# Kernel tuning notes

Measured on AMD Instinct MI355X. Metric: run time of the kernel, lower is better.

The kernel has to match this reference:

```python
import jax, jax.numpy as jnp
import numpy as np
from jax import lax

B, H, W = 1024, 28, 28
STEPS, KMAX = 32, 2
OUT_F, NUM_CLASSES = 32, 10
P = H * W  # 784 flattened filtration values
TSEQ1 = jnp.linspace(0.01, 0.29, STEPS, dtype=jnp.float32)
TSEQ2 = jnp.linspace(0.05, 0.3, STEPS, dtype=jnp.float32)
DN = ('NHWC', 'HWIO', 'NHWC')


def setup_inputs() -> dict:
    key = jax.random.key(0)
    ks = jax.random.split(key, 16)
    return {
        'x': jax.random.normal(ks[0], (B, H, W, 1), jnp.float32),
        'x_dtm005': jax.random.uniform(ks[1], (B, H, W, 1), jnp.float32, 0.0, 0.3),
        'x_dtm02': jax.random.uniform(ks[2], (B, H, W, 1), jnp.float32, 0.0, 0.3),
        'conv_w1': jax.random.normal(ks[3], (3, 3, 1, 32), jnp.float32) * 0.1,
        'conv_b1': jnp.zeros((32,), jnp.float32),
        'conv_w2': jax.random.normal(ks[4], (3, 3, 32, 1), jnp.float32) * 0.1,
        'conv_b2': jnp.zeros((1,), jnp.float32),
        'g1_w': jax.random.normal(ks[5], (KMAX * STEPS, OUT_F), jnp.float32) * 0.1,
        'g1_b': jnp.zeros((OUT_F,), jnp.float32),
        'g2_w': jax.random.normal(ks[6], (KMAX * STEPS, OUT_F), jnp.float32) * 0.1,
        'g2_b': jnp.zeros((OUT_F,), jnp.float32),
        'fc1_w': jax.random.normal(ks[7], (P + 2 * OUT_F, 64), jnp.float32) * 0.05,
        'fc1_b': jnp.zeros((64,), jnp.float32),
        'fc2_w': jax.random.normal(ks[8], (64, NUM_CLASSES), jnp.float32) * 0.1,
        'fc2_b': jnp.zeros((NUM_CLASSES,), jnp.float32),
    }


def _landscape(v, tseq):
    """Persistence landscape over a grid of t-values.

    v: [B, P] filtration (DTM) values; each value is a birth time, paired
    with a per-sample death at the max filtration value (sublevel sweep).
    Landscape lambda_k(t) = k-th largest tent max(0, min(t-b, d-t)).
    Returns [B, KMAX*STEPS].
    """
    death = jnp.max(v, axis=1)                                     # [B]
    # tent: [B, T, P]
    tent = jnp.maximum(0.0, jnp.minimum(tseq[None, :, None] - v[:, None, :],
                                        death[:, None, None] - tseq[None, :, None]))
    top = lax.top_k(tent, KMAX)[0]                                 # [B, T, K]
    return jnp.transpose(top, (0, 2, 1)).reshape(v.shape[0], KMAX * tseq.shape[0])


def reference(x, x_dtm005, x_dtm02, conv_w1, conv_b1, conv_w2, conv_b2,
              g1_w, g1_b, g2_w, g2_b, fc1_w, fc1_b, fc2_w, fc2_b):
    b = x.shape[0]
    # TDA branch 1 (sublevel=True -> no negation)
    x1 = _landscape(x_dtm005.reshape(b, -1), TSEQ1)
    x1 = jax.nn.relu(x1 @ g1_w + g1_b)
    # TDA branch 2
    x2 = _landscape(x_dtm02.reshape(b, -1), TSEQ2)
    x2 = jax.nn.relu(x2 @ g2_w + g2_b)
    # CNN branch: Conv(32) -> ReLU -> Conv(1), then extra ReLU per call()
    h = lax.conv_general_dilated(x, conv_w1, (1, 1), 'SAME', dimension_numbers=DN) + conv_b1
    h = jax.nn.relu(h)
    h = lax.conv_general_dilated(h, conv_w2, (1, 1), 'SAME', dimension_numbers=DN) + conv_b2
    h = jax.nn.relu(h)
    hf = h.reshape(b, -1)                                          # [B, 784]
    z = jnp.concatenate([hf, x1, x2], axis=-1)                     # [B, 848]
    z = jax.nn.relu(z @ fc1_w + fc1_b)
    return z @ fc2_w + fc2_b                                       # [B, 10]
```

## Files before the change

### kernel.cpp

```cpp
#include <hip/hip_runtime.h>

#define BATCH 1024
#define PP 784

__global__ __launch_bounds__(256) void fused_kernel(
    const float* __restrict__ xin,
    const float* __restrict__ dtm1, const float* __restrict__ dtm2,
    const float* __restrict__ w1g, const float* __restrict__ b1g,
    const float* __restrict__ w2g, const float* __restrict__ b2g,
    const float* __restrict__ g1w, const float* __restrict__ g1b,
    const float* __restrict__ g2w, const float* __restrict__ g2b,
    const float* __restrict__ fc1w, const float* __restrict__ fc1b,
    const float* __restrict__ fc2w, const float* __restrict__ fc2b,
    float* __restrict__ out)
{
  const int b = blockIdx.x;
  const int tid = threadIdx.x;
  const int lane = tid & 63;
  const int w = tid >> 6;
  const int x = lane & 31;
  const int sub = lane >> 5;

  __shared__ float inL[28][36];
  __shared__ float w1L[9][32];
  __shared__ float w2L[9][32];
  __shared__ float b1L[32];
  __shared__ float pL[4][28][28];
  __shared__ __align__(16) float zL[864];
  __shared__ float red[2][4][3];
  __shared__ float fin[2][3];
  __shared__ float pfc[4][64];
  __shared__ float z1L[64];

  float4 tv1, tv2;
  if (tid < 196) {
    tv1 = *(const float4*)&dtm1[b * PP + tid * 4];
    tv2 = *(const float4*)&dtm2[b * PP + tid * 4];
  }

  for (int i = tid; i < 224; i += 256) {
    int y = i >> 3, k = i & 7;
    inL[y][k == 0 ? 0 : 28 + k] = 0.f;
  }
  for (int i = tid; i < 784; i += 256)
    inL[i / 28][i % 28 + 1] = xin[b * PP + i];
  for (int i = tid; i < 288; i += 256) {
    ((float*)w1L)[i] = w1g[i];
    ((float*)w2L)[i] = w2g[i];
  }
  if (tid < 32) b1L[tid] = b1g[tid];
  __syncthreads();

  float acc[28];
#pragma unroll
  for (int y = 0; y < 28; ++y) acc[y] = 0.f;

#pragma unroll 1
  for (int cp = 0; cp < 4; ++cp) {
    const int c = (w << 3) + (cp << 1) + sub;
    float wa[9], wb[9];
#pragma unroll
    for (int t = 0; t < 9; ++t) { wa[t] = w1L[t][c]; wb[t] = w2L[t][c]; }
    const float bb = b1L[c];

    float ra0 = 0.f, ra1 = 0.f, ra2 = 0.f;
    float rb0 = inL[0][x], rb1 = inL[0][x + 1], rb2 = inL[0][x + 2];

#pragma unroll
    for (int y = 0; y < 28; ++y) {
      float rc0, rc1, rc2;
      if (y + 1 < 28) {
        rc0 = inL[y + 1][x]; rc1 = inL[y + 1][x + 1]; rc2 = inL[y + 1][x + 2];
      } else {
        rc0 = 0.f; rc1 = 0.f; rc2 = 0.f;
      }
      float h = bb;
      h = fmaf(ra0, wa[0], h); h = fmaf(ra1, wa[1], h); h = fmaf(ra2, wa[2], h);
      h = fmaf(rb0, wa[3], h); h = fmaf(rb1, wa[4], h); h = fmaf(rb2, wa[5], h);
      h = fmaf(rc0, wa[6], h); h = fmaf(rc1, wa[7], h); h = fmaf(rc2, wa[8], h);
      h = (x < 28) ? fmaxf(h, 0.f) : 0.f;
      float hl = __shfl_up(h, 1, 32);  hl = (x == 0) ? 0.f : hl;
      float hr = __shfl_down(h, 1, 32);
      if (y + 1 < 28) {
        acc[y + 1] = fmaf(hl, wb[0], acc[y + 1]);
        acc[y + 1] = fmaf(h , wb[1], acc[y + 1]);
        acc[y + 1] = fmaf(hr, wb[2], acc[y + 1]);
      }
      acc[y] = fmaf(hl, wb[3], acc[y]);
      acc[y] = fmaf(h , wb[4], acc[y]);
      acc[y] = fmaf(hr, wb[5], acc[y]);
      if (y > 0) {
        acc[y - 1] = fmaf(hl, wb[6], acc[y - 1]);
        acc[y - 1] = fmaf(h , wb[7], acc[y - 1]);
        acc[y - 1] = fmaf(hr, wb[8], acc[y - 1]);
      }
      ra0 = rb0; ra1 = rb1; ra2 = rb2;
      rb0 = rc0; rb1 = rc1; rb2 = rc2;
    }
  }
#pragma unroll
  for (int y = 0; y < 28; ++y) acc[y] += __shfl_xor(acc[y], 32);
  if (sub == 0 && x < 28) {
#pragma unroll
    for (int y = 0; y < 28; ++y) pL[w][y][x] = acc[y];
  }
  __syncthreads();

  {
    const float b2v = b2g[0];
    const float* pw = (const float*)pL;
    for (int u = tid; u < 784; u += 256) {
      float v = pw[u] + pw[784 + u] + pw[1568 + u] + pw[2352 + u] + b2v;
      zL[u] = fmaxf(v, 0.f);
    }
  }
#pragma unroll
  for (int br = 0; br < 2; ++br) {
    float m1 = 1e30f, m2 = 1e30f, mx = -1e30f;
    if (tid < 196) {
      float4 x4 = br ? tv2 : tv1;
      float xs[4] = {x4.x, x4.y, x4.z, x4.w};
#pragma unroll
      for (int k = 0; k < 4; ++k) {
        float v = xs[k];
        mx = fmaxf(mx, v);
        float nm1 = fminf(m1, v);
        m2 = fminf(m2, fmaxf(m1, v));
        m1 = nm1;
      }
    }
#pragma unroll
    for (int off = 32; off >= 1; off >>= 1) {
      float o1 = __shfl_xor(m1, off);
      float o2 = __shfl_xor(m2, off);
      float ox = __shfl_xor(mx, off);
      mx = fmaxf(mx, ox);
      float nm1 = fminf(m1, o1);
      m2 = fminf(fminf(m2, o2), fmaxf(m1, o1));
      m1 = nm1;
    }
    if ((tid & 63) == 0) {
      red[br][w][0] = m1; red[br][w][1] = m2; red[br][w][2] = mx;
    }
  }
  __syncthreads();
  if (tid < 2) {
    float m1 = 1e30f, m2 = 1e30f, mx = -1e30f;
#pragma unroll
    for (int wv = 0; wv < 4; ++wv) {
      float o1 = red[tid][wv][0], o2 = red[tid][wv][1], ox = red[tid][wv][2];
      mx = fmaxf(mx, ox);
      float nm1 = fminf(m1, o1);
      m2 = fminf(fminf(m2, o2), fmaxf(m1, o1));
      m1 = nm1;
    }
    fin[tid][0] = m1; fin[tid][1] = m2; fin[tid][2] = mx;
  }
  __syncthreads();
  if (tid < 64) {
    const int br = tid >> 5, j = tid & 31;
    const float m1 = fin[br][0], m2 = fin[br][1], mx = fin[br][2];
    const float* gw = br ? g2w : g1w;
    const float* gb = br ? g2b : g1b;
    const float t0 = br ? 0.05f : 0.01f;
    const float dt = br ? (0.25f / 31.0f) : (0.28f / 31.0f);
    float a = gb[j];
#pragma unroll 4
    for (int i = 0; i < 64; ++i) {
      const int k = i >> 5, ti = i & 31;
      float tv = t0 + dt * (float)ti;
      float vk = k ? m2 : m1;
      float lam = fmaxf(0.0f, fminf(tv - vk, mx - tv));
      a = fmaf(lam, gw[i * 32 + j], a);
    }
    zL[784 + br * 32 + j] = fmaxf(a, 0.0f);
  }
  __syncthreads();

  {
    const int j = tid & 63, part = tid >> 6;
    float a = 0.f;
    const int i0 = part * 212;
#pragma unroll 4
    for (int i = i0; i < i0 + 212; i += 4) {
      float4 z4 = *(float4*)&zL[i];
      a = fmaf(z4.x, fc1w[(i + 0) * 64 + j], a);
      a = fmaf(z4.y, fc1w[(i + 1) * 64 + j], a);
      a = fmaf(z4.z, fc1w[(i + 2) * 64 + j], a);
      a = fmaf(z4.w, fc1w[(i + 3) * 64 + j], a);
    }
    pfc[part][j] = a;
  }
  __syncthreads();
  if (tid < 64) {
    float v = pfc[0][tid] + pfc[1][tid] + pfc[2][tid] + pfc[3][tid] + fc1b[tid];
    z1L[tid] = fmaxf(v, 0.f);
  }
  __syncthreads();
  if (tid < 10) {
    float a = fc2b[tid];
#pragma unroll 8
    for (int jj = 0; jj < 64; ++jj)
      a = fmaf(z1L[jj], fc2w[jj * 10 + tid], a);
    out[b * 10 + tid] = a;
  }
}

extern "C" void kernel_launch(void* const* d_in, const int* in_sizes, int n_in,
                              void* d_out, int out_size, void* d_ws, size_t ws_size,
                              hipStream_t stream) {
  const float* x       = (const float*)d_in[0];
  const float* dtm005  = (const float*)d_in[1];
  const float* dtm02   = (const float*)d_in[2];
  const float* conv_w1 = (const float*)d_in[3];
  const float* conv_b1 = (const float*)d_in[4];
  const float* conv_w2 = (const float*)d_in[5];
  const float* conv_b2 = (const float*)d_in[6];
  const float* g1_w    = (const float*)d_in[7];
  const float* g1_b    = (const float*)d_in[8];
  const float* g2_w    = (const float*)d_in[9];
  const float* g2_b    = (const float*)d_in[10];
  const float* fc1_w   = (const float*)d_in[11];
  const float* fc1_b   = (const float*)d_in[12];
  const float* fc2_w   = (const float*)d_in[13];
  const float* fc2_b   = (const float*)d_in[14];
  float* out = (float*)d_out;

  fused_kernel<<<BATCH, 256, 0, stream>>>(
      x, dtm005, dtm02, conv_w1, conv_b1, conv_w2, conv_b2,
      g1_w, g1_b, g2_w, g2_b, fc1_w, fc1_b, fc2_w, fc2_b, out);
}
```

Before: 128.5 us.

## Restructure fused conv to stream rows with rolling accumulators and DPP shifts

```diff
diff --git a/kernel.cpp b/kernel.cpp
--- a/kernel.cpp
+++ b/kernel.cpp
@@ -3,7 +3,16 @@
 #define BATCH 1024
 #define PP 784
 
-__global__ __launch_bounds__(256) void fused_kernel(
+__device__ __forceinline__ float dpp_wave_shr1(float v) {
+  return __int_as_float(__builtin_amdgcn_update_dpp(
+      0, __float_as_int(v), 0x138, 0xF, 0xF, true));
+}
+__device__ __forceinline__ float dpp_wave_shl1(float v) {
+  return __int_as_float(__builtin_amdgcn_update_dpp(
+      0, __float_as_int(v), 0x130, 0xF, 0xF, true));
+}
+
+__global__ __launch_bounds__(256, 4) void fused_kernel(
     const float* __restrict__ xin,
     const float* __restrict__ dtm1, const float* __restrict__ dtm2,
     const float* __restrict__ w1g, const float* __restrict__ b1g,
@@ -16,21 +25,16 @@
 {
   const int b = blockIdx.x;
   const int tid = threadIdx.x;
+  const int w = tid >> 6;
   const int lane = tid & 63;
-  const int w = tid >> 6;
   const int x = lane & 31;
-  const int sub = lane >> 5;
 
   __shared__ float inL[28][36];
-  __shared__ float w1L[9][32];
-  __shared__ float w2L[9][32];
+  __shared__ __align__(16) float wTL[2][32][12];
   __shared__ float b1L[32];
-  __shared__ float pL[4][28][28];
+  __shared__ __align__(16) float pL[8][28][28];
   __shared__ __align__(16) float zL[864];
   __shared__ float red[2][4][3];
-  __shared__ float fin[2][3];
-  __shared__ float pfc[4][64];
-  __shared__ float z1L[64];
 
   float4 tv1, tv2;
   if (tid < 196) {
@@ -45,64 +49,58 @@
   for (int i = tid; i < 784; i += 256)
     inL[i / 28][i % 28 + 1] = xin[b * PP + i];
   for (int i = tid; i < 288; i += 256) {
-    ((float*)w1L)[i] = w1g[i];
-    ((float*)w2L)[i] = w2g[i];
+    int c = i & 31, t = i >> 5;
+    wTL[0][c][t] = w1g[i];
+    wTL[1][c][t] = w2g[i];
   }
   if (tid < 32) b1L[tid] = b1g[tid];
   __syncthreads();
 
-  float acc[28];
-#pragma unroll
-  for (int y = 0; y < 28; ++y) acc[y] = 0.f;
-
-#pragma unroll 1
-  for (int cp = 0; cp < 4; ++cp) {
-    const int c = (w << 3) + (cp << 1) + sub;
-    float wa[9], wb[9];
-#pragma unroll
-    for (int t = 0; t < 9; ++t) { wa[t] = w1L[t][c]; wb[t] = w2L[t][c]; }
-    const float bb = b1L[c];
-
-    float ra0 = 0.f, ra1 = 0.f, ra2 = 0.f;
-    float rb0 = inL[0][x], rb1 = inL[0][x + 1], rb2 = inL[0][x + 2];
-
-#pragma unroll
+  {
+    const int sub = lane >> 5;
+    const int slot = tid >> 5;
+    float4 waA[4], waB[4], wbA[4], wbB[4];
+    float wa8[4], wb8[4], bb[4];
+#pragma unroll
+    for (int cp = 0; cp < 4; ++cp) {
+      const int c = (w << 3) + (cp << 1) + sub;
+      const float* p1 = &wTL[0][c][0];
+      const float* p2 = &wTL[1][c][0];
+      waA[cp] = *(const float4*)p1; waB[cp] = *(const float4*)(p1 + 4); wa8[cp] = p1[8];
+      wbA[cp] = *(const float4*)p2; wbB[cp] = *(const float4*)(p2 + 4); wb8[cp] = p2[8];
+      bb[cp] = b1L[c];
+    }
+
+    float A0 = 0.f, A1 = 0.f, A2 = 0.f;
+    float B0 = inL[0][x], B1 = inL[0][x + 1], B2 = inL[0][x + 2];
+    float aM = 0.f, aC = 0.f, aP = 0.f;
+
+#pragma unroll 2
     for (int y = 0; y < 28; ++y) {
-      float rc0, rc1, rc2;
-      if (y + 1 < 28) {
-        rc0 = inL[y + 1][x]; rc1 = inL[y + 1][x + 1]; rc2 = inL[y + 1][x + 2];
-      } else {
-        rc0 = 0.f; rc1 = 0.f; rc2 = 0.f;
+      float C0, C1, C2;
+      if (y < 27) {
+        C0 = inL[y + 1][x]; C1 = inL[y + 1][x + 1]; C2 = inL[y + 1][x + 2];
+      } else { C0 = 0.f; C1 = 0.f; C2 = 0.f; }
+
+#pragma unroll
+      for (int cp = 0; cp < 4; ++cp) {
+        float h = bb[cp];
+        h = fmaf(A0, waA[cp].x, h); h = fmaf(A1, waA[cp].y, h); h = fmaf(A2, waA[cp].z, h);
+        h = fmaf(B0, waA[cp].w, h); h = fmaf(B1, waB[cp].x, h); h = fmaf(B2, waB[cp].y, h);
+        h = fmaf(C0, waB[cp].z, h); h = fmaf(C1, waB[cp].w, h); h = fmaf(C2, wa8[cp], h);
+        h = (x < 28) ? fmaxf(h, 0.f) : 0.f;
+        float hl = dpp_wave_shr1(h);
+        float hr = dpp_wave_shl1(h);
+        aP = fmaf(hl, wbA[cp].x, aP); aP = fmaf(h, wbA[cp].y, aP); aP = fmaf(hr, wbA[cp].z, aP);
+        aC = fmaf(hl, wbA[cp].w, aC); aC = fmaf(h, wbB[cp].x, aC); aC = fmaf(hr, wbB[cp].y, aC);
+        aM = fmaf(hl, wbB[cp].z, aM); aM = fmaf(h, wbB[cp].w, aM); aM = fmaf(hr, wb8[cp], aM);
       }
-      float h = bb;
-      h = fmaf(ra0, wa[0], h); h = fmaf(ra1, wa[1], h); h = fmaf(ra2, wa[2], h);
-      h = fmaf(rb0, wa[3], h); h = fmaf(rb1, wa[4], h); h = fmaf(rb2, wa[5], h);
-      h = fmaf(rc0, wa[6], h); h = fmaf(rc1, wa[7], h); h = fmaf(rc2, wa[8], h);
-      h = (x < 28) ? fmaxf(h, 0.f) : 0.f;
-      float hl = __shfl_up(h, 1, 32);  hl = (x == 0) ? 0.f : hl;
-      float hr = __shfl_down(h, 1, 32);
-      if (y + 1 < 28) {
-        acc[y + 1] = fmaf(hl, wb[0], acc[y + 1]);
-        acc[y + 1] = fmaf(h , wb[1], acc[y + 1]);
-        acc[y + 1] = fmaf(hr, wb[2], acc[y + 1]);
-      }
-      acc[y] = fmaf(hl, wb[3], acc[y]);
-      acc[y] = fmaf(h , wb[4], acc[y]);
-      acc[y] = fmaf(hr, wb[5], acc[y]);
-      if (y > 0) {
-        acc[y - 1] = fmaf(hl, wb[6], acc[y - 1]);
-        acc[y - 1] = fmaf(h , wb[7], acc[y - 1]);
-        acc[y - 1] = fmaf(hr, wb[8], acc[y - 1]);
-      }
-      ra0 = rb0; ra1 = rb1; ra2 = rb2;
-      rb0 = rc0; rb1 = rc1; rb2 = rc2;
-    }
-  }
-#pragma unroll
-  for (int y = 0; y < 28; ++y) acc[y] += __shfl_xor(acc[y], 32);
-  if (sub == 0 && x < 28) {
-#pragma unroll
-    for (int y = 0; y < 28; ++y) pL[w][y][x] = acc[y];
+      if (y > 0 && x < 28) pL[slot][y - 1][x] = aM;
+      aM = aC; aC = aP; aP = 0.f;
+      A0 = B0; A1 = B1; A2 = B2;
+      B0 = C0; B1 = C1; B2 = C2;
+    }
+    if (x < 28) pL[slot][27][x] = aM;
   }
   __syncthreads();
 
@@ -110,7 +108,8 @@
     const float b2v = b2g[0];
     const float* pw = (const float*)pL;
     for (int u = tid; u < 784; u += 256) {
-      float v = pw[u] + pw[784 + u] + pw[1568 + u] + pw[2352 + u] + b2v;
+      float v = pw[u] + pw[784 + u] + pw[1568 + u] + pw[2352 + u]
+              + pw[3136 + u] + pw[3920 + u] + pw[4704 + u] + pw[5488 + u] + b2v;
       zL[u] = fmaxf(v, 0.f);
     }
   }
@@ -144,22 +143,18 @@
     }
   }
   __syncthreads();
-  if (tid < 2) {
+
+  if (tid < 64) {
+    const int br = tid >> 5, j = tid & 31;
     float m1 = 1e30f, m2 = 1e30f, mx = -1e30f;
 #pragma unroll
     for (int wv = 0; wv < 4; ++wv) {
-      float o1 = red[tid][wv][0], o2 = red[tid][wv][1], ox = red[tid][wv][2];
+      float o1 = red[br][wv][0], o2 = red[br][wv][1], ox = red[br][wv][2];
       mx = fmaxf(mx, ox);
       float nm1 = fminf(m1, o1);
       m2 = fminf(fminf(m2, o2), fmaxf(m1, o1));
       m1 = nm1;
     }
-    fin[tid][0] = m1; fin[tid][1] = m2; fin[tid][2] = mx;
-  }
-  __syncthreads();
-  if (tid < 64) {
-    const int br = tid >> 5, j = tid & 31;
-    const float m1 = fin[br][0], m2 = fin[br][1], mx = fin[br][2];
     const float* gw = br ? g2w : g1w;
     const float* gb = br ? g2b : g1b;
     const float t0 = br ? 0.05f : 0.01f;
@@ -177,32 +172,35 @@
   }
   __syncthreads();
 
-  {
-    const int j = tid & 63, part = tid >> 6;
-    float a = 0.f;
-    const int i0 = part * 212;
-#pragma unroll 4
-    for (int i = i0; i < i0 + 212; i += 4) {
-      float4 z4 = *(float4*)&zL[i];
-      a = fmaf(z4.x, fc1w[(i + 0) * 64 + j], a);
-      a = fmaf(z4.y, fc1w[(i + 1) * 64 + j], a);
-      a = fmaf(z4.z, fc1w[(i + 2) * 64 + j], a);
-      a = fmaf(z4.w, fc1w[(i + 3) * 64 + j], a);
-    }
-    pfc[part][j] = a;
-  }
-  __syncthreads();
-  if (tid < 64) {
-    float v = pfc[0][tid] + pfc[1][tid] + pfc[2][tid] + pfc[3][tid] + fc1b[tid];
-    z1L[tid] = fmaxf(v, 0.f);
-  }
-  __syncthreads();
-  if (tid < 10) {
-    float a = fc2b[tid];
+  float* pfcF = &pL[0][0][0];
+  {
+    const int part = tid >> 4, jq = tid & 15;
+    float ax = 0.f, ay = 0.f, az = 0.f, aw = 0.f;
+    const int i0 = part * 53;
+    for (int i = i0; i < i0 + 53; ++i) {
+      float zv = zL[i];
+      float4 w4 = *(const float4*)&fc1w[i * 64 + jq * 4];
+      ax = fmaf(zv, w4.x, ax); ay = fmaf(zv, w4.y, ay);
+      az = fmaf(zv, w4.z, az); aw = fmaf(zv, w4.w, aw);
+    }
+    *(float4*)&pfcF[part * 64 + jq * 4] = make_float4(ax, ay, az, aw);
+  }
+  __syncthreads();
+  {
+    float* z1L = pfcF + 1024;
+    if (tid < 64) {
+      float v = fc1b[tid];
+#pragma unroll
+      for (int p = 0; p < 16; ++p) v += pfcF[p * 64 + tid];
+      z1L[tid] = fmaxf(v, 0.f);
+    }
+    if (tid < 10) {
+      float a = fc2b[tid];
 #pragma unroll 8
-    for (int jj = 0; jj < 64; ++jj)
-      a = fmaf(z1L[jj], fc2w[jj * 10 + tid], a);
-    out[b * 10 + tid] = a;
+      for (int jj = 0; jj < 64; ++jj)
+        a = fmaf(z1L[jj], fc2w[jj * 10 + tid], a);
+      out[b * 10 + tid] = a;
+    }
   }
 }
 
```

Result: faster. 112.7 us (-12.3%).
